# Performance work log

Hardware: AMD Instinct MI355X
Metric: run time of the kernel (lower is better)

Reference implementation:

```python
import jax, jax.numpy as jnp
import numpy as np

# OPT-1.3b-like attention dims
B, S, E, NH, HD = 1, 2048, 2048, 32, 64
Q_BITS, R_BITS, BASE_GS, R_GS = 1, 3, 16, 16


def quotrem_fake_quantize(x, q_bits=Q_BITS, r_bits=R_BITS, base_gs=BASE_GS, r_gs=R_GS):
    r_max = 2 ** (r_bits - 1) - 1
    r_min = -r_max - 1
    eps = 1e-8
    shape = x.shape
    H = shape[-1]
    xg = x.reshape(shape[:-1] + (H // base_gs, base_gs))  # [..., G_base, base_gs]
    max_abs = jnp.maximum(jnp.max(jnp.abs(xg), axis=-1, keepdims=True), eps)
    if q_bits == 1:
        log2_max = jnp.log2(max_abs)
        base_floor = jnp.exp2(jnp.floor(log2_max))
        base_ceil = jnp.exp2(jnp.ceil(log2_max))
        base = jnp.where(jnp.abs(max_abs - base_floor) <= jnp.abs(base_ceil - max_abs),
                         base_floor, base_ceil)
        base = jnp.clip(base, 1.0, 128.0)
        max_pos = jnp.max(xg, axis=-1, keepdims=True)
        min_val = jnp.min(xg, axis=-1, keepdims=True)
        sign_flag = jnp.where(jnp.abs(max_pos) >= jnp.abs(min_val), 1.0, -1.0)
        q = (xg * sign_flag >= base / 2.0).astype(x.dtype)
        q_scaled = q * sign_flag * base
    else:
        q_max = 2 ** (q_bits - 1) - 1
        threshold = max_abs / q_max
        base = jnp.full_like(threshold, 64.0)
        for b in (32.0, 16.0, 8.0, 4.0, 2.0):
            base = jnp.where(threshold <= b, jnp.full_like(threshold, b), base)
        q = jnp.clip(jnp.round(xg / base), -q_max, q_max)
        q_scaled = q * base
    r = (xg - q_scaled).reshape(shape)
    rg = r.reshape(shape[:-1] + (H // r_gs, r_gs))  # [..., G_r, r_gs]
    max_abs_r = jnp.maximum(jnp.max(jnp.abs(rg), axis=-1, keepdims=True), eps)
    scale_r = max_abs_r / r_max
    r_q = jnp.clip(jnp.round(rg / scale_r), r_min, r_max)
    r_dq = (r_q * scale_r).reshape(shape)
    return q_scaled.reshape(shape) + r_dq


def setup_inputs() -> dict:
    key = jax.random.key(0)
    ks = jax.random.split(key, 9)
    w = lambda k: jax.random.normal(k, (E, E), dtype=jnp.float32) * 0.02
    b = lambda k: jax.random.normal(k, (E,), dtype=jnp.float32) * 0.02
    return {
        "hidden_states": jax.random.normal(ks[0], (B, S, E), dtype=jnp.float32),
        "Wq": w(ks[1]), "bq": b(ks[2]),
        "Wk": w(ks[3]), "bk": b(ks[4]),
        "Wv": w(ks[5]), "bv": b(ks[6]),
        "Wo": w(ks[7]), "bo": b(ks[8]),
    }


def reference(hidden_states, Wq, bq, Wk, bk, Wv, bv, Wo, bo):
    scaling = HD ** -0.5
    heads = lambda x: x.reshape(B, S, NH, HD).transpose(0, 2, 1, 3)  # [B,NH,S,HD]
    q = heads((hidden_states @ Wq.T + bq) * scaling)
    k = quotrem_fake_quantize(heads(hidden_states @ Wk.T + bk))
    v = quotrem_fake_quantize(heads(hidden_states @ Wv.T + bv))
    scores = jnp.einsum('bhqd,bhkd->bhqk', q, k)
    idx = jnp.arange(S)
    scores = jnp.where(idx[:, None] >= idx[None, :], scores, -jnp.inf)  # causal
    attn = jax.nn.softmax(scores, axis=-1)
    out = jnp.einsum('bhqk,bhkd->bhqd', attn, v).transpose(0, 2, 1, 3).reshape(B, S, E)
    return out @ Wo.T + bo
```

## Files before the change

### kernel.cpp

```cpp
#include <hip/hip_runtime.h>
#include <math.h>

#define SEQ 2048
#define EMB 2048
#define NHEAD 32
#define HDIM 64

typedef unsigned short u16;
typedef _Float16 half8 __attribute__((ext_vector_type(8)));
typedef _Float16 half4 __attribute__((ext_vector_type(4)));
typedef __attribute__((ext_vector_type(4))) float floatx4;

__device__ __forceinline__ floatx4 mfma_f16(half8 a, half8 b, floatx4 c) {
    return __builtin_amdgcn_mfma_f32_16x16x32_f16(a, b, c, 0, 0, 0);
}
__device__ __forceinline__ void load16(const u16* g, u16* l) {
    __builtin_amdgcn_global_load_lds(
        (const __attribute__((address_space(1))) unsigned int*)g,
        (__attribute__((address_space(3))) unsigned int*)l, 16, 0, 0);
}
__device__ __forceinline__ u16 h2u(_Float16 h) { return *reinterpret_cast<u16*>(&h); }

__global__ __launch_bounds__(256)
void cvt4(const float* __restrict__ X0, u16* __restrict__ Y0,
          const float* __restrict__ X1, u16* __restrict__ Y1,
          const float* __restrict__ X2, u16* __restrict__ Y2,
          const float* __restrict__ X3, u16* __restrict__ Y3)
{
    const float* Xs[4] = {X0, X1, X2, X3};
    u16* Ys[4] = {Y0, Y1, Y2, Y3};
    const float* X = Xs[blockIdx.y];
    u16* Y = Ys[blockIdx.y];
    const int i = (blockIdx.x * 256 + threadIdx.x) * 4;
    float4 v = *reinterpret_cast<const float4*>(X + i);
    half4 hv;
    hv.x = (_Float16)v.x; hv.y = (_Float16)v.y;
    hv.z = (_Float16)v.z; hv.w = (_Float16)v.w;
    *reinterpret_cast<half4*>(Y + i) = hv;
}

__global__ __launch_bounds__(512, 2)
void gemm256(const u16* __restrict__ A,
             const u16* __restrict__ B0, const u16* __restrict__ B1,
             const u16* __restrict__ B2,
             const float* __restrict__ bk, const float* __restrict__ bv,
             const float* __restrict__ bq,
             const float* __restrict__ Wo, u16* __restrict__ Wo16,
             float* __restrict__ F0, float* __restrict__ F1,
             u16* __restrict__ Qb)
{
    __shared__ __align__(16) u16 As[2][256 * 64];
    __shared__ __align__(16) u16 Bs[2][256 * 64];

    const int tid = threadIdx.x;
    const int bn = blockIdx.x, bm = blockIdx.y, z = blockIdx.z;

    if (z == 3) {
        const int b = bm * 8 + bn;
        #pragma unroll
        for (int c = 0; c < 32; ++c) {
            const int i = ((c * 64 + b) * 512 + tid) * 4;
            float4 v = *reinterpret_cast<const float4*>(Wo + i);
            half4 hv;
            hv.x = (_Float16)v.x; hv.y = (_Float16)v.y;
            hv.z = (_Float16)v.z; hv.w = (_Float16)v.w;
            *reinterpret_cast<half4*>(Wo16 + i) = hv;
        }
        return;
    }

    const int w = tid >> 6, lane = tid & 63;
    const int wm = w >> 2, wn = w & 3;
    const int quad = lane >> 4, colk = lane & 15;
    const int lrow = lane >> 3, lphy = lane & 7;
    const int lsLog = (lphy - lrow) & 7;

    const u16* Bg  = (z == 0) ? B0 : (z == 1) ? B1 : B2;
    const u16* Ag  = A  + (size_t)(bm * 256 + lrow) * EMB + lsLog * 8;
    const u16* Bgp = Bg + (size_t)(bn * 256 + lrow) * EMB + lsLog * 8;

    const int kp0 = ((quad + colk) & 7) * 8;
    const int kp1 = ((quad + 4 + colk) & 7) * 8;
    int arow[8], brow[4];
    #pragma unroll
    for (int i = 0; i < 8; ++i) arow[i] = (wm * 128 + 16 * i + colk) * 64;
    #pragma unroll
    for (int j = 0; j < 4; ++j) brow[j] = (wn * 64 + 16 * j + colk) * 64;

    floatx4 acc[8][4];
    #pragma unroll
    for (int i = 0; i < 8; ++i)
        #pragma unroll
        for (int j = 0; j < 4; ++j) acc[i][j] = (floatx4){0.f, 0.f, 0.f, 0.f};

#define STAGE_A(MQ, BUF, KT) {                                                \
    _Pragma("unroll") for (int p_ = 0; p_ < 2; ++p_) {                        \
        const int r0_ = 128 * p_ + (MQ) * 64 + w * 8;                         \
        load16(Ag + (size_t)r0_ * EMB + (KT), &As[BUF][r0_ * 64 + lane * 8]); \
    } }
#define STAGE_B(NQ, BUF, KT) {                                                \
    _Pragma("unroll") for (int p_ = 0; p_ < 2; ++p_) {                        \
        const int b_ = w + 8 * p_;                                            \
        const int r0_ = 64 * (b_ >> 2) + (NQ) * 32 + (b_ & 3) * 8;            \
        load16(Bgp + (size_t)r0_ * EMB + (KT), &Bs[BUF][r0_ * 64 + lane * 8]);\
    } }

#define PHASE(MQ, NQ, BUF, STAGE, GUARD) {                                    \
    half8 af[4][2], bf[2][2];                                                 \
    _Pragma("unroll") for (int ii = 0; ii < 4; ++ii) {                        \
        const u16* ap_ = &As[BUF][arow[4 * (MQ) + ii]];                       \
        af[ii][0] = *reinterpret_cast<const half8*>(ap_ + kp0);               \
        af[ii][1] = *reinterpret_cast<const half8*>(ap_ + kp1);               \
    }                                                                         \
    _Pragma("unroll") for (int jj = 0; jj < 2; ++jj) {                        \
        const u16* bp_ = &Bs[BUF][brow[2 * (NQ) + jj]];                       \
        bf[jj][0] = *reinterpret_cast<const half8*>(bp_ + kp0);               \
        bf[jj][1] = *reinterpret_cast<const half8*>(bp_ + kp1);               \
    }                                                                         \
    STAGE                                                                     \
    __builtin_amdgcn_s_barrier();                                             \
    asm volatile("s_waitcnt lgkmcnt(0)" ::: "memory");                        \
    __builtin_amdgcn_s_setprio(1);                                            \
    _Pragma("unroll") for (int ii = 0; ii < 4; ++ii)                          \
        _Pragma("unroll") for (int jj = 0; jj < 2; ++jj) {                    \
            acc[4*(MQ)+ii][2*(NQ)+jj] =                                       \
                mfma_f16(af[ii][0], bf[jj][0], acc[4*(MQ)+ii][2*(NQ)+jj]);    \
            acc[4*(MQ)+ii][2*(NQ)+jj] =                                       \
                mfma_f16(af[ii][1], bf[jj][1], acc[4*(MQ)+ii][2*(NQ)+jj]);    \
        }                                                                     \
    __builtin_amdgcn_s_setprio(0);                                            \
    if (GUARD) asm volatile("s_waitcnt vmcnt(4)" ::: "memory");               \
    __builtin_amdgcn_s_barrier();                                             \
    __builtin_amdgcn_sched_barrier(0);                                        \
}

    STAGE_B(0, 0, 0)
    STAGE_A(0, 0, 0)
    STAGE_A(1, 0, 0)
    STAGE_B(1, 0, 0)
    STAGE_B(0, 1, 64)
    STAGE_A(0, 1, 64)
    asm volatile("s_waitcnt vmcnt(4)" ::: "memory");
    __builtin_amdgcn_s_barrier();
    __builtin_amdgcn_sched_barrier(0);

    #pragma unroll 1
    for (int it = 0; it < 16; ++it) {
        const int k1 = ((2 * it + 1) & 31) * 64;
        const int k2 = ((2 * it + 2) & 31) * 64;
        const int k3 = ((2 * it + 3) & 31) * 64;
        PHASE(0, 0, 0, STAGE_A(1, 1, k1), 0)
        PHASE(1, 0, 0, STAGE_B(1, 1, k1), 0)
        PHASE(0, 1, 0, STAGE_B(0, 0, k2), 0)
        PHASE(1, 1, 0, STAGE_A(0, 0, k2), 1)
        PHASE(0, 0, 1, STAGE_A(1, 0, k2), 0)
        PHASE(1, 0, 1, STAGE_B(1, 0, k2), 0)
        PHASE(0, 1, 1, STAGE_B(0, 1, k3), 0)
        PHASE(1, 1, 1, STAGE_A(0, 1, k3), 1)
    }
    asm volatile("s_waitcnt vmcnt(0)" ::: "memory");

#undef STAGE_A
#undef STAGE_B
#undef PHASE

    const float* bias = (z == 0) ? bk : (z == 1) ? bv : bq;
    #pragma unroll
    for (int i = 0; i < 8; ++i) {
        const int row = bm * 256 + wm * 128 + 16 * i + 4 * quad;
        #pragma unroll
        for (int j = 0; j < 4; ++j) {
            const int col = bn * 256 + wn * 64 + 16 * j + colk;
            const float bb = bias[col];
            #pragma unroll
            for (int r = 0; r < 4; ++r) {
                const size_t idx = (size_t)(row + r) * EMB + col;
                if (z == 2)
                    ((_Float16*)Qb)[idx] = (_Float16)((acc[i][j][r] + bb) * 0.125f);
                else
                    ((z == 0) ? F0 : F1)[idx] = acc[i][j][r] + bb;
            }
        }
    }
}

__global__ __launch_bounds__(256)
void gemm16(const u16* __restrict__ A,
            const u16* __restrict__ B0, const u16* __restrict__ B1,
            const u16* __restrict__ B2,
            const float* __restrict__ bk, const float* __restrict__ bv,
            const float* __restrict__ bq,
            float* __restrict__ F0, float* __restrict__ F1,
            u16* __restrict__ Qb)
{
    __shared__ __align__(16) u16 As[128 * 64];
    __shared__ __align__(16) u16 Bs[128 * 64];

    const int tid = threadIdx.x;
    const int w = tid >> 6, lane = tid & 63;
    const int quad = lane >> 4, colk = lane & 15;
    const int bn = blockIdx.x, bm = blockIdx.y, z = blockIdx.z;
    const int wm = (w & 1) * 64, wn = (w >> 1) * 64;

    const u16* Bg = (z == 0) ? B0 : (z == 1) ? B1 : B2;

    const int srow = tid >> 3, sphy = tid & 7;
    const int sLog = (sphy - srow) & 7;
    size_t agof[4], bgof[4];
    int ldst[4];
    #pragma unroll
    for (int p = 0; p < 4; ++p) {
        const int row = srow + 32 * p;
        agof[p] = (size_t)(bm * 128 + row) * EMB + sLog * 8;
        bgof[p] = (size_t)(bn * 128 + row) * EMB + sLog * 8;
        ldst[p] = (tid + 256 * p) * 8;
    }

    const int aoct0 = ((quad + colk) & 7) * 8;
    const int aoct1 = ((quad + 4 + colk) & 7) * 8;

    floatx4 acc[4][4];
    #pragma unroll
    for (int i = 0; i < 4; ++i)
        #pragma unroll
        for (int j = 0; j < 4; ++j) acc[i][j] = (floatx4){0.f, 0.f, 0.f, 0.f};

    for (int kt = 0; kt < 2048; kt += 64) {
        __syncthreads();
        #pragma unroll
        for (int p = 0; p < 4; ++p) {
            load16(A  + agof[p] + kt, As + ldst[p]);
            load16(Bg + bgof[p] + kt, Bs + ldst[p]);
        }
        __syncthreads();

        half8 a0[4], a1[4], b0[4], b1[4];
        #pragma unroll
        for (int i = 0; i < 4; ++i) {
            a0[i] = *reinterpret_cast<const half8*>(&As[(wm + 16*i + colk) * 64 + aoct0]);
            a1[i] = *reinterpret_cast<const half8*>(&As[(wm + 16*i + colk) * 64 + aoct1]);
        }
        #pragma unroll
        for (int j = 0; j < 4; ++j) {
            b0[j] = *reinterpret_cast<const half8*>(&Bs[(wn + 16*j + colk) * 64 + aoct0]);
            b1[j] = *reinterpret_cast<const half8*>(&Bs[(wn + 16*j + colk) * 64 + aoct1]);
        }
        #pragma unroll
        for (int i = 0; i < 4; ++i)
            #pragma unroll
            for (int j = 0; j < 4; ++j) {
                acc[i][j] = mfma_f16(a0[i], b0[j], acc[i][j]);
                acc[i][j] = mfma_f16(a1[i], b1[j], acc[i][j]);
            }
    }

    const float* bias = (z == 0) ? bk : (z == 1) ? bv : bq;
    #pragma unroll
    for (int i = 0; i < 4; ++i) {
        const int row = bm * 128 + wm + 16*i + 4*quad;
        #pragma unroll
        for (int j = 0; j < 4; ++j) {
            const int col = bn * 128 + wn + 16*j + colk;
            const float bv2 = bias[col];
            #pragma unroll
            for (int r = 0; r < 4; ++r) {
                const size_t idx = (size_t)(row + r) * EMB + col;
                if (z == 2)
                    ((_Float16*)Qb)[idx] = (_Float16)((acc[i][j][r] + bv2) * 0.125f);
                else
                    ((z == 0) ? F0 : F1)[idx] = acc[i][j][r] + bv2;
            }
        }
    }
}

__device__ __forceinline__ void quotrem16(float* x)
{
    float maxabs = 1e-8f, maxpos = -INFINITY, minval = INFINITY;
    #pragma unroll
    for (int i = 0; i < 16; ++i) {
        maxabs = fmaxf(maxabs, fabsf(x[i]));
        maxpos = fmaxf(maxpos, x[i]);
        minval = fminf(minval, x[i]);
    }
    const float lg = log2f(maxabs);
    const float bfl = exp2f(floorf(lg));
    const float bcl = exp2f(ceilf(lg));
    float base = (fabsf(maxabs - bfl) <= fabsf(bcl - maxabs)) ? bfl : bcl;
    base = fminf(fmaxf(base, 1.0f), 128.0f);
    const float sgn = (fabsf(maxpos) >= fabsf(minval)) ? 1.0f : -1.0f;
    const float hb = 0.5f * base, sb = sgn * base;

    float qs[16], r[16], maxr = 1e-8f;
    #pragma unroll
    for (int i = 0; i < 16; ++i) {
        qs[i] = (x[i] * sgn >= hb) ? sb : 0.0f;
        r[i]  = x[i] - qs[i];
        maxr  = fmaxf(maxr, fabsf(r[i]));
    }
    const float scale = maxr / 3.0f;
    #pragma unroll
    for (int i = 0; i < 16; ++i) {
        float rq = rintf(r[i] / scale);
        rq = fminf(fmaxf(rq, -4.0f), 3.0f);
        x[i] = qs[i] + rq * scale;
    }
}

__global__ __launch_bounds__(256)
void quant_kv(const float* __restrict__ FK, u16* __restrict__ Kb,
              const float* __restrict__ FV, u16* __restrict__ Vt)
{
    __shared__ u16 T[64 * 264];
    const int bid = blockIdx.x, t = threadIdx.x;

    if (bid < 1024) {
        const int g = bid * 256 + t;
        const float* p = FK + (size_t)g * 16;
        float x[16];
        #pragma unroll
        for (int i = 0; i < 16; i += 4)
            *reinterpret_cast<float4*>(&x[i]) = *reinterpret_cast<const float4*>(p + i);
        quotrem16(x);
        half8 h0, h1;
        #pragma unroll
        for (int i = 0; i < 8; ++i) {
            h0[i] = (_Float16)x[i];
            h1[i] = (_Float16)x[8 + i];
        }
        u16* o = Kb + (size_t)g * 16;
        *reinterpret_cast<half8*>(o) = h0;
        *reinterpret_cast<half8*>(o + 8) = h1;
        return;
    }

    const int l = bid - 1024;
    const int sb = l >> 5, h = l & 31;
    const float* src = FV + (size_t)(sb * 256 + t) * EMB + h * HDIM;

    #pragma unroll
    for (int g4 = 0; g4 < 4; ++g4) {
        float x[16];
        #pragma unroll
        for (int i = 0; i < 16; i += 4)
            *reinterpret_cast<float4*>(&x[i]) =
                *reinterpret_cast<const float4*>(src + g4 * 16 + i);
        quotrem16(x);
        #pragma unroll
        for (int i = 0; i < 16; ++i)
            T[(g4 * 16 + i) * 264 + t] = h2u((_Float16)x[i]);
    }
    __syncthreads();

    const int d = t >> 2, seg = t & 3;
    u16* dst = Vt + (size_t)(h * HDIM + d) * SEQ + sb * 256 + seg * 64;
    #pragma unroll
    for (int jj = 0; jj < 8; ++jj)
        *reinterpret_cast<half8*>(dst + jj * 8) =
            *reinterpret_cast<const half8*>(&T[d * 264 + seg * 64 + jj * 8]);
}

__global__ __launch_bounds__(512)
void flash128(const u16* __restrict__ Qb, const u16* __restrict__ Kb,
              const u16* __restrict__ Vt, u16* __restrict__ Ob)
{
    __shared__ __align__(16) u16 Ks[2][128 * 64];
    __shared__ __align__(16) u16 Vs[2][64 * 128];
    __shared__ __align__(16) u16 Ps[128 * 136];

    const int tid = threadIdx.x;
    const int w = tid >> 6, lane = tid & 63;
    const int wg = w >> 2, wl = w & 3;
    const int quad = lane >> 4, colk = lane & 15;
    const int id = blockIdx.x;
    const int h = (id & 7) * 4 + ((id >> 3) & 3);
    const int pairb = id >> 5;

    int krow[2], koff[2], vd[2], voff[2], ldst[2];
    #pragma unroll
    for (int p = 0; p < 2; ++p) {
        const int c = tid + p * 512;
        krow[p] = c >> 3;
        koff[p] = (((c & 7) - krow[p]) & 7) * 8;
        vd[p]   = c >> 4;
        voff[p] = (((c & 15) - vd[p]) & 15) * 8;
        ldst[p] = c * 8;
    }
    const int kp0 = ((quad + colk) & 7) * 8;
    const int kp1 = ((quad + 4 + colk) & 7) * 8;
    const int rloc = wg * 64 + 16 * wl + colk;

#define STAGEKV(KW, BUF) {                                                     \
    _Pragma("unroll") for (int p_ = 0; p_ < 2; ++p_) {                         \
        load16(Kb + (size_t)((KW) * 128 + krow[p_]) * EMB + h * HDIM + koff[p_],\
               &Ks[BUF][ldst[p_]]);                                            \
        load16(Vt + (size_t)(h * HDIM + vd[p_]) * SEQ + (KW) * 128 + voff[p_], \
               &Vs[BUF][ldst[p_]]);                                            \
    } }

    #pragma unroll
    for (int pass = 0; pass < 2; ++pass) {
        const int qt = pass ? (15 - pairb) : pairb;
        const int nw = qt + 1;
        const int qrow_g = qt * 128 + rloc;

        const half8 qb0 = *reinterpret_cast<const half8*>(
            &Qb[(size_t)qrow_g * EMB + h * HDIM + quad * 8]);
        const half8 qb1 = *reinterpret_cast<const half8*>(
            &Qb[(size_t)qrow_g * EMB + h * HDIM + 32 + quad * 8]);

        STAGEKV(0, 0)

        floatx4 o[4];
        #pragma unroll
        for (int t = 0; t < 4; ++t) o[t] = (floatx4){0.f, 0.f, 0.f, 0.f};
        float lsum = 0.f;
        int cur = 0;

        #pragma unroll 1
        for (int kw = 0; kw < nw; ++kw) {
            if (kw + 1 < nw) {
                STAGEKV(kw + 1, cur ^ 1)
                asm volatile("s_waitcnt vmcnt(4)" ::: "memory");
            } else {
                asm volatile("s_waitcnt vmcnt(0)" ::: "memory");
            }
            __builtin_amdgcn_s_barrier();
            __builtin_amdgcn_sched_barrier(0);

            floatx4 s[8];
            __builtin_amdgcn_s_setprio(1);
            #pragma unroll
            for (int t = 0; t < 8; ++t) {
                const half8 kb0 = *reinterpret_cast<const half8*>(&Ks[cur][(16*t + colk) * 64 + kp0]);
                const half8 kb1 = *reinterpret_cast<const half8*>(&Ks[cur][(16*t + colk) * 64 + kp1]);
                floatx4 zz = (floatx4){0.f, 0.f, 0.f, 0.f};
                zz = mfma_f16(kb0, qb0, zz);
                s[t] = mfma_f16(kb1, qb1, zz);
            }
            __builtin_amdgcn_s_setprio(0);
            if (kw == nw - 1) {
                #pragma unroll
                for (int t = 0; t < 8; ++t)
                    #pragma unroll
                    for (int r = 0; r < 4; ++r)
                        if (kw * 128 + 16*t + 4*quad + r > qrow_g) s[t][r] = -INFINITY;
            }

            #pragma unroll
            for (int t = 0; t < 8; ++t) {
                half4 pw;
                float pv0 = __expf(s[t][0] - 4.0f), pv1 = __expf(s[t][1] - 4.0f);
                float pv2 = __expf(s[t][2] - 4.0f), pv3 = __expf(s[t][3] - 4.0f);
                lsum += (pv0 + pv1) + (pv2 + pv3);
                pw.x = (_Float16)pv0; pw.y = (_Float16)pv1;
                pw.z = (_Float16)pv2; pw.w = (_Float16)pv3;
                *reinterpret_cast<half4*>(&Ps[rloc * 136 + 16*t + 4*quad]) = pw;
            }

            half8 pa[4];
            #pragma unroll
            for (int seg = 0; seg < 4; ++seg)
                pa[seg] = *reinterpret_cast<const half8*>(&Ps[rloc * 136 + seg * 32 + quad * 8]);
            __builtin_amdgcn_s_setprio(1);
            #pragma unroll
            for (int t = 0; t < 4; ++t) {
                #pragma unroll
                for (int seg = 0; seg < 4; ++seg) {
                    const int vp = ((4*seg + quad + colk) & 15) * 8;
                    const half8 vb = *reinterpret_cast<const half8*>(&Vs[cur][(16*t + colk) * 128 + vp]);
                    o[t] = mfma_f16(pa[seg], vb, o[t]);
                }
            }
            __builtin_amdgcn_s_setprio(0);

            __builtin_amdgcn_s_barrier();
            __builtin_amdgcn_sched_barrier(0);
            cur ^= 1;
        }

        lsum += __shfl_xor(lsum, 16, 64);
        lsum += __shfl_xor(lsum, 32, 64);

        float invr[4];
        #pragma unroll
        for (int r = 0; r < 4; ++r) invr[r] = 1.0f / __shfl(lsum, 4*quad + r, 64);
        #pragma unroll
        for (int t = 0; t < 4; ++t)
            #pragma unroll
            for (int r = 0; r < 4; ++r) {
                const int row = qt * 128 + wg * 64 + 16*wl + 4*quad + r;
                ((_Float16*)Ob)[(size_t)row * EMB + h * HDIM + 16*t + colk] =
                    (_Float16)(o[t][r] * invr[r]);
            }
    }
#undef STAGEKV
}

extern "C" void kernel_launch(void* const* d_in, const int* in_sizes, int n_in,
                              void* d_out, int out_size, void* d_ws, size_t ws_size,
                              hipStream_t stream)
{
    const float* hidden = (const float*)d_in[0];
    const float* Wq = (const float*)d_in[1];
    const float* bq = (const float*)d_in[2];
    const float* Wk = (const float*)d_in[3];
    const float* bk = (const float*)d_in[4];
    const float* Wv = (const float*)d_in[5];
    const float* bv = (const float*)d_in[6];
    const float* Wo = (const float*)d_in[7];
    const float* bo = (const float*)d_in[8];
    float* out = (float*)d_out;

    char* ws = (char*)d_ws;
    const size_t MB = 1024 * 1024;
    u16*   H16  = (u16*)(ws);
    u16*   Wk16 = (u16*)(ws + 8 * MB);
    u16*   Wv16 = (u16*)(ws + 16 * MB);
    float* FK   = (float*)(ws + 24 * MB);
    float* FV   = (float*)(ws + 40 * MB);
    u16*   Wo16 = (u16*)(ws + 56 * MB);
    u16*   Kbuf = (u16*)(ws + 8 * MB);
    u16*   Vtb  = (u16*)(ws + 16 * MB);
    u16*   Obuf = (u16*)(ws + 24 * MB);
    u16*   Wq16 = (u16*)d_out;
    u16*   Qbuf = (u16*)((char*)d_out + 8 * MB);

    const dim3 cb(256);
    float* nilf = nullptr; u16* nil16 = nullptr;

    hipLaunchKernelGGL(cvt4, dim3(4096, 4), cb, 0, stream,
                       hidden, H16, Wk, Wk16, Wv, Wv16, Wq, Wq16);
    hipLaunchKernelGGL(gemm256, dim3(8, 8, 4), dim3(512), 0, stream,
                       H16, Wk16, Wv16, Wq16, bk, bv, bq,
                       Wo, Wo16, FK, FV, Qbuf);
    hipLaunchKernelGGL(quant_kv, dim3(1280), cb, 0, stream,
                       FK, Kbuf, FV, Vtb);
    hipLaunchKernelGGL(flash128, dim3(256), dim3(512), 0, stream,
                       Qbuf, Kbuf, Vtb, Obuf);
    hipLaunchKernelGGL(gemm16, dim3(16, 16, 1), cb, 0, stream,
                       Obuf, Wo16, nil16, nil16, bo, nilf, nilf,
                       out, nilf, nil16);
}
```

Baseline: 292.2 us.

## Merge GEMM mainloop phases to halve barriers and reuse B fragments

The QKV projection GEMM mainloop goes from eight phases per iteration to four. Each phase now runs 32 MFMAs over the full N width and stages two global-to-LDS loads instead of one. B fragments are read from LDS once per buffer and reused across both M halves, which cuts LDS read traffic and the number of block barriers and priority switches per K step. In exchange, more fragment registers stay live and the software-pipeline schedule gets coarser, so there is less room to overlap loads with MFMA work.

```diff
diff --git a/kernel.cpp b/kernel.cpp
--- a/kernel.cpp
+++ b/kernel.cpp
@@ -92,6 +92,8 @@
     for (int i = 0; i < 8; ++i)
         #pragma unroll
         for (int j = 0; j < 4; ++j) acc[i][j] = (floatx4){0.f, 0.f, 0.f, 0.f};
+
+    half8 af[4][2], bf0[2][2], bf1[2][2];
 
 #define STAGE_A(MQ, BUF, KT) {                                                \
     _Pragma("unroll") for (int p_ = 0; p_ < 2; ++p_) {                        \
@@ -104,42 +106,50 @@
         const int r0_ = 64 * (b_ >> 2) + (NQ) * 32 + (b_ & 3) * 8;            \
         load16(Bgp + (size_t)r0_ * EMB + (KT), &Bs[BUF][r0_ * 64 + lane * 8]);\
     } }
-
-#define PHASE(MQ, NQ, BUF, STAGE, GUARD) {                                    \
-    half8 af[4][2], bf[2][2];                                                 \
-    _Pragma("unroll") for (int ii = 0; ii < 4; ++ii) {                        \
-        const u16* ap_ = &As[BUF][arow[4 * (MQ) + ii]];                       \
-        af[ii][0] = *reinterpret_cast<const half8*>(ap_ + kp0);               \
-        af[ii][1] = *reinterpret_cast<const half8*>(ap_ + kp1);               \
-    }                                                                         \
-    _Pragma("unroll") for (int jj = 0; jj < 2; ++jj) {                        \
-        const u16* bp_ = &Bs[BUF][brow[2 * (NQ) + jj]];                       \
-        bf[jj][0] = *reinterpret_cast<const half8*>(bp_ + kp0);               \
-        bf[jj][1] = *reinterpret_cast<const half8*>(bp_ + kp1);               \
-    }                                                                         \
-    STAGE                                                                     \
+#define READ_A(MQ, BUF)                                                       \
+    _Pragma("unroll") for (int ii_ = 0; ii_ < 4; ++ii_) {                     \
+        const u16* ap_ = &As[BUF][arow[4*(MQ)+ii_]];                          \
+        af[ii_][0] = *reinterpret_cast<const half8*>(ap_ + kp0);              \
+        af[ii_][1] = *reinterpret_cast<const half8*>(ap_ + kp1);              \
+    }
+#define READ_B2(BUF)                                                          \
+    _Pragma("unroll") for (int jj_ = 0; jj_ < 2; ++jj_) {                     \
+        const u16* b0_ = &Bs[BUF][brow[jj_]];                                 \
+        bf0[jj_][0] = *reinterpret_cast<const half8*>(b0_ + kp0);             \
+        bf0[jj_][1] = *reinterpret_cast<const half8*>(b0_ + kp1);             \
+        const u16* b1_ = &Bs[BUF][brow[2+jj_]];                               \
+        bf1[jj_][0] = *reinterpret_cast<const half8*>(b1_ + kp0);             \
+        bf1[jj_][1] = *reinterpret_cast<const half8*>(b1_ + kp1);             \
+    }
+
+#define PHASE2(MQ, RD, STG, GUARD) {                                          \
+    RD                                                                        \
+    STG                                                                       \
     __builtin_amdgcn_s_barrier();                                             \
     asm volatile("s_waitcnt lgkmcnt(0)" ::: "memory");                        \
     __builtin_amdgcn_s_setprio(1);                                            \
-    _Pragma("unroll") for (int ii = 0; ii < 4; ++ii)                          \
+    _Pragma("unroll") for (int ii = 0; ii < 4; ++ii) {                        \
         _Pragma("unroll") for (int jj = 0; jj < 2; ++jj) {                    \
-            acc[4*(MQ)+ii][2*(NQ)+jj] =                                       \
-                mfma_f16(af[ii][0], bf[jj][0], acc[4*(MQ)+ii][2*(NQ)+jj]);    \
-            acc[4*(MQ)+ii][2*(NQ)+jj] =                                       \
-                mfma_f16(af[ii][1], bf[jj][1], acc[4*(MQ)+ii][2*(NQ)+jj]);    \
+            acc[4*(MQ)+ii][jj] =                                              \
+                mfma_f16(af[ii][0], bf0[jj][0], acc[4*(MQ)+ii][jj]);          \
+            acc[4*(MQ)+ii][jj] =                                              \
+                mfma_f16(af[ii][1], bf0[jj][1], acc[4*(MQ)+ii][jj]);          \
         }                                                                     \
+        _Pragma("unroll") for (int jj = 0; jj < 2; ++jj) {                    \
+            acc[4*(MQ)+ii][2+jj] =                                            \
+                mfma_f16(af[ii][0], bf1[jj][0], acc[4*(MQ)+ii][2+jj]);        \
+            acc[4*(MQ)+ii][2+jj] =                                            \
+                mfma_f16(af[ii][1], bf1[jj][1], acc[4*(MQ)+ii][2+jj]);        \
+        }                                                                     \
+    }                                                                         \
     __builtin_amdgcn_s_setprio(0);                                            \
     if (GUARD) asm volatile("s_waitcnt vmcnt(4)" ::: "memory");               \
     __builtin_amdgcn_s_barrier();                                             \
     __builtin_amdgcn_sched_barrier(0);                                        \
 }
 
-    STAGE_B(0, 0, 0)
-    STAGE_A(0, 0, 0)
-    STAGE_A(1, 0, 0)
-    STAGE_B(1, 0, 0)
-    STAGE_B(0, 1, 64)
-    STAGE_A(0, 1, 64)
+    STAGE_A(0, 0, 0)  STAGE_B(0, 0, 0)  STAGE_A(1, 0, 0)  STAGE_B(1, 0, 0)
+    STAGE_A(0, 1, 64) STAGE_B(0, 1, 64)
     asm volatile("s_waitcnt vmcnt(4)" ::: "memory");
     __builtin_amdgcn_s_barrier();
     __builtin_amdgcn_sched_barrier(0);
@@ -149,20 +159,18 @@
         const int k1 = ((2 * it + 1) & 31) * 64;
         const int k2 = ((2 * it + 2) & 31) * 64;
         const int k3 = ((2 * it + 3) & 31) * 64;
-        PHASE(0, 0, 0, STAGE_A(1, 1, k1), 0)
-        PHASE(1, 0, 0, STAGE_B(1, 1, k1), 0)
-        PHASE(0, 1, 0, STAGE_B(0, 0, k2), 0)
-        PHASE(1, 1, 0, STAGE_A(0, 0, k2), 1)
-        PHASE(0, 0, 1, STAGE_A(1, 0, k2), 0)
-        PHASE(1, 0, 1, STAGE_B(1, 0, k2), 0)
-        PHASE(0, 1, 1, STAGE_B(0, 1, k3), 0)
-        PHASE(1, 1, 1, STAGE_A(0, 1, k3), 1)
+        PHASE2(0, READ_A(0,0) READ_B2(0), STAGE_A(1,1,k1) STAGE_B(1,1,k1), 0)
+        PHASE2(1, READ_A(1,0),            STAGE_A(0,0,k2) STAGE_B(0,0,k2), 1)
+        PHASE2(0, READ_A(0,1) READ_B2(1), STAGE_A(1,0,k2) STAGE_B(1,0,k2), 0)
+        PHASE2(1, READ_A(1,1),            STAGE_A(0,1,k3) STAGE_B(0,1,k3), 1)
     }
     asm volatile("s_waitcnt vmcnt(0)" ::: "memory");
 
 #undef STAGE_A
 #undef STAGE_B
-#undef PHASE
+#undef READ_A
+#undef READ_B2
+#undef PHASE2
 
     const float* bias = (z == 0) ? bk : (z == 1) ? bv : bq;
     #pragma unroll
```

Result: faster. 284.0 us (-2.8%).
